# Kernel tuning notes

Hardware: AMD Instinct MI355X
Metric: run time of the kernel (lower is better)

## Reference

```python
import jax, jax.numpy as jnp
import numpy as np

D_MODEL = 1024
N_HEADS = 8
HEAD_DIM = D_MODEL // N_HEADS
B, T = 4, 2048


def setup_inputs() -> dict:
    key = jax.random.key(0)
    ks = jax.random.split(key, 10)
    x = jax.random.normal(ks[0], (B, T, D_MODEL), dtype=jnp.float32)
    # causal mask: True entries are masked (matches torch masked_fill semantics)
    mask = jnp.triu(jnp.ones((T, T), dtype=bool), k=1)

    def xavier(k, shape):
        fan_in, fan_out = shape[1], shape[0]
        lim = float(np.sqrt(6.0 / (fan_in + fan_out)))
        return jax.random.uniform(k, shape, jnp.float32, -lim, lim)

    Wq = xavier(ks[1], (D_MODEL, D_MODEL)); bq = jnp.zeros((D_MODEL,), jnp.float32)
    Wk = xavier(ks[2], (D_MODEL, D_MODEL)); bk = jnp.zeros((D_MODEL,), jnp.float32)
    Wv = xavier(ks[3], (D_MODEL, D_MODEL)); bv = jnp.zeros((D_MODEL,), jnp.float32)
    Wo = xavier(ks[4], (D_MODEL, D_MODEL)); bo = jnp.zeros((D_MODEL,), jnp.float32)
    return {"x": x, "mask": mask, "Wq": Wq, "bq": bq, "Wk": Wk, "bk": bk,
            "Wv": Wv, "bv": bv, "Wo": Wo, "bo": bo}


def reference(x, mask, Wq, bq, Wk, bk, Wv, bv, Wo, bo):
    Bsz, Tlen, _ = x.shape
    # torch Linear: y = x @ W.T + b
    Q = (x @ Wq.T + bq).reshape(Bsz, Tlen, N_HEADS, HEAD_DIM).transpose(0, 2, 1, 3)  # [B,H,T,Dh]
    K = (x @ Wk.T + bk).reshape(Bsz, Tlen, N_HEADS, HEAD_DIM).transpose(0, 2, 1, 3)  # [B,H,T,Dh]
    V_shared = x @ Wv.T + bv  # [B,T,D] shared across heads
    scale = 1.0 / jnp.sqrt(jnp.float32(HEAD_DIM))
    scores = jnp.einsum('bhqd,bhkd->bhqk', Q, K) * scale  # [B,H,T,T]
    scores = jnp.where(mask[None, None, :, :], jnp.float32(-1e9), scores)
    attn_per_head = jax.nn.softmax(scores, axis=-1)
    alpha_agg = attn_per_head.mean(axis=1)  # [B,T,T] head-averaged attention
    out = jnp.einsum('bqk,bkd->bqd', alpha_agg, V_shared) @ Wo.T + bo
    return out, alpha_agg
```

## Files before the change

### kernel.cpp

```cpp
#include <hip/hip_runtime.h>
#include <hip/hip_bf16.h>

#define D_MODEL 1024
#define NH 8
#define HD 128
#define BATCH 4
#define TSEQ 2048
#define MROWS (BATCH * TSEQ)

typedef __attribute__((ext_vector_type(8))) __bf16 bf16x8;
typedef __attribute__((ext_vector_type(4))) __bf16 bf16x4;
typedef __attribute__((ext_vector_type(4))) float f32x4;
typedef __attribute__((ext_vector_type(8))) unsigned short u16x8;

__device__ __forceinline__ void gload16(const void* g, void* lds) {
  __builtin_amdgcn_global_load_lds(
      (const __attribute__((address_space(1))) unsigned int*)g,
      (__attribute__((address_space(3))) unsigned int*)lds, 16, 0, 0);
}

__global__ __launch_bounds__(256) void cvt_f32_to_bf16(const float* __restrict__ in,
                                                       __bf16* __restrict__ out, int n4) {
  int i = blockIdx.x * 256 + threadIdx.x;
  if (i < n4) {
    float4 v = reinterpret_cast<const float4*>(in)[i];
    bf16x4 o;
    o[0] = (__bf16)v.x; o[1] = (__bf16)v.y; o[2] = (__bf16)v.z; o[3] = (__bf16)v.w;
    reinterpret_cast<bf16x4*>(out)[i] = o;
  }
}

template <bool BF16OUT, bool CAUSAL, bool AFP32>
__global__ __launch_bounds__(256) void gemm128(const void* __restrict__ Aip,
                                               const __bf16* __restrict__ Bp,
                                               const float* __restrict__ bias,
                                               void* __restrict__ Yp, int K, int ldy,
                                               size_t sA, size_t sB, size_t sY) {
  __shared__ __bf16 As[128 * 32];
  __shared__ __bf16 Bs[128 * 32];
  const int tid = threadIdx.x;
  const int w = tid >> 6, l = tid & 63;
  const int lr = l & 15, lg = l >> 4;
  const int m0 = blockIdx.y * 128, n0 = blockIdx.x * 128;
  const int z = blockIdx.z;
  const __bf16* Ab = AFP32 ? nullptr : (const __bf16*)Aip + z * sA;
  const float* Af = AFP32 ? (const float*)Aip + z * sA : nullptr;
  const __bf16* Bb = Bp + z * sB;
  const int wm = w >> 1, wn = w & 1;
  f32x4 acc[4][4] = {};
  const int Klim = CAUSAL ? (m0 + 128 < K ? m0 + 128 : K) : K;

  for (int k0 = 0; k0 < Klim; k0 += 32) {
    if (k0) __syncthreads();
    if constexpr (!AFP32) {
#pragma unroll
      for (int i = 0; i < 2; ++i) {
        int s = w * 128 + i * 64 + l;
        int row = s >> 2, scp = s & 3;
        int sc = scp ^ ((row >> 1) & 3);
        gload16(Ab + (size_t)(m0 + row) * K + k0 + sc * 8, (char*)As + s * 16);
      }
    } else {
#pragma unroll
      for (int i = 0; i < 2; ++i) {
        int s = w * 128 + i * 64 + l;
        int row = s >> 2, sc = s & 3;
        const float* src = Af + (size_t)(m0 + row) * K + k0 + sc * 8;
        float4 lo = *reinterpret_cast<const float4*>(src);
        float4 hi = *reinterpret_cast<const float4*>(src + 4);
        bf16x8 v;
        v[0] = (__bf16)lo.x; v[1] = (__bf16)lo.y; v[2] = (__bf16)lo.z; v[3] = (__bf16)lo.w;
        v[4] = (__bf16)hi.x; v[5] = (__bf16)hi.y; v[6] = (__bf16)hi.z; v[7] = (__bf16)hi.w;
        int p = row * 4 + (sc ^ ((row >> 1) & 3));
        *reinterpret_cast<bf16x8*>((char*)As + p * 16) = v;
      }
    }
#pragma unroll
    for (int i = 0; i < 2; ++i) {
      int s = w * 128 + i * 64 + l;
      int row = s >> 2, scp = s & 3;
      int sc = scp ^ ((row >> 1) & 3);
      gload16(Bb + (size_t)(n0 + row) * K + k0 + sc * 8, (char*)Bs + s * 16);
    }
    __syncthreads();
    bf16x8 af[4], bf[4];
#pragma unroll
    for (int f = 0; f < 4; ++f) {
      int ar = wm * 64 + f * 16 + lr;
      af[f] = *reinterpret_cast<const bf16x8*>((const char*)As + ar * 64 +
                                               ((lg ^ ((ar >> 1) & 3)) * 16));
      int br = wn * 64 + f * 16 + lr;
      bf[f] = *reinterpret_cast<const bf16x8*>((const char*)Bs + br * 64 +
                                               ((lg ^ ((br >> 1) & 3)) * 16));
    }
#pragma unroll
    for (int mf = 0; mf < 4; ++mf)
#pragma unroll
      for (int nf = 0; nf < 4; ++nf)
        acc[mf][nf] = __builtin_amdgcn_mfma_f32_16x16x32_bf16(af[mf], bf[nf], acc[mf][nf], 0, 0, 0);
  }

#pragma unroll
  for (int mf = 0; mf < 4; ++mf) {
#pragma unroll
    for (int nf = 0; nf < 4; ++nf) {
#pragma unroll
      for (int r = 0; r < 4; ++r) {
        int grow = m0 + wm * 64 + mf * 16 + lg * 4 + r;
        int gcol = n0 + wn * 64 + nf * 16 + lr;
        float v = acc[mf][nf][r];
        if (bias) v += bias[gcol];
        if constexpr (BF16OUT)
          ((__bf16*)Yp + z * sY)[(size_t)grow * ldy + gcol] = (__bf16)v;
        else
          ((float*)Yp + z * sY)[(size_t)grow * ldy + gcol] = v;
      }
    }
  }
}

__global__ __launch_bounds__(256) void transpose_v(const __bf16* __restrict__ V,
                                                   __bf16* __restrict__ Vt) {
  __shared__ unsigned short tile[64 * 72];
  const int b = blockIdx.z;
  const int t0 = blockIdx.x * 64, d0 = blockIdx.y * 64;
  const int tid = threadIdx.x;
#pragma unroll
  for (int i = 0; i < 2; ++i) {
    int s = i * 256 + tid;
    int r = s >> 3, c8 = s & 7;
    u16x8 v = *reinterpret_cast<const u16x8*>(V + ((size_t)b * TSEQ + t0 + r) * D_MODEL + d0 + c8 * 8);
    *reinterpret_cast<u16x8*>(&tile[r * 72 + c8 * 8]) = v;
  }
  __syncthreads();
#pragma unroll
  for (int i = 0; i < 2; ++i) {
    int s = i * 256 + tid;
    int dr = s >> 3, t8 = s & 7;
    u16x8 o;
#pragma unroll
    for (int j = 0; j < 8; ++j) o[j] = tile[(t8 * 8 + j) * 72 + dr];
    *reinterpret_cast<u16x8*>(Vt + ((size_t)b * D_MODEL + d0 + dr) * TSEQ + t0 + t8 * 8) = o;
  }
}

#define STAGE_QK(srcbase, dst)                                                    \
  {                                                                               \
    _Pragma("unroll") for (int i = 0; i < 4; ++i) {                               \
      int s = w * 256 + i * 64 + l;                                               \
      int row = s >> 4, sp = s & 15;                                              \
      int sc = sp ^ (row & 7);                                                    \
      gload16((srcbase) + (size_t)row * D_MODEL + sc * 8, (char*)(dst) + s * 16); \
    }                                                                             \
  }

__device__ __forceinline__ bf16x8 ld_tile(const __bf16* t, int row, int c, int lg) {
  return *reinterpret_cast<const bf16x8*>((const char*)t + row * 256 +
                                          (((c * 4 + lg) ^ (row & 7)) * 16));
}

__global__ __launch_bounds__(256) void attn_stats(const __bf16* __restrict__ Q,
                                                  const __bf16* __restrict__ Kp,
                                                  float* __restrict__ Linv) {
  __shared__ __bf16 Qs[64 * 128];
  __shared__ __bf16 Ks[64 * 128];
  const int tid = threadIdx.x;
  const int w = tid >> 6, l = tid & 63;
  const int lr = l & 15, lg = l >> 4;
  const int qt = blockIdx.x, q0 = qt * 64;
  const int b = blockIdx.y >> 3, h = blockIdx.y & 7;
  const float scale = 0.08838834764831845f;

  const __bf16* qsrc = Q + ((size_t)(b * TSEQ + q0)) * D_MODEL + h * HD;
  STAGE_QK(qsrc, Qs);

  bf16x8 af[4];
  float lsum[4] = {0.f, 0.f, 0.f, 0.f};
  const int nkt = qt + 1;
  for (int kt = 0; kt < nkt; ++kt) {
    if (kt) __syncthreads();
    const __bf16* ksrc = Kp + ((size_t)(b * TSEQ + kt * 64)) * D_MODEL + h * HD;
    STAGE_QK(ksrc, Ks);
    __syncthreads();
    if (kt == 0) {
      int qrow = w * 16 + lr;
#pragma unroll
      for (int c = 0; c < 4; ++c) af[c] = ld_tile(Qs, qrow, c, lg);
    }
#pragma unroll
    for (int kf = 0; kf < 4; ++kf) {
      f32x4 acc = {};
      int krow = kf * 16 + lr;
#pragma unroll
      for (int c = 0; c < 4; ++c)
        acc = __builtin_amdgcn_mfma_f32_16x16x32_bf16(af[c], ld_tile(Ks, krow, c, lg), acc, 0, 0, 0);
      if (kt == qt) {
#pragma unroll
        for (int r = 0; r < 4; ++r) {
          int q = q0 + w * 16 + lg * 4 + r;
          int k = kt * 64 + kf * 16 + lr;
          if (k <= q) lsum[r] += __expf(acc[r] * scale);
        }
      } else {
#pragma unroll
        for (int r = 0; r < 4; ++r) lsum[r] += __expf(acc[r] * scale);
      }
    }
  }
#pragma unroll
  for (int m = 1; m < 16; m <<= 1)
#pragma unroll
    for (int r = 0; r < 4; ++r) lsum[r] += __shfl_xor(lsum[r], m, 64);
  if (lr == 0) {
#pragma unroll
    for (int r = 0; r < 4; ++r)
      Linv[((size_t)(b * NH + h)) * TSEQ + q0 + w * 16 + lg * 4 + r] =
          1.0f / ((float)NH * lsum[r]);
  }
}

__global__ __launch_bounds__(256) void attn_alpha(const __bf16* __restrict__ Q,
                                                  const __bf16* __restrict__ Kp,
                                                  const float* __restrict__ Linv,
                                                  float* __restrict__ alpha) {
  const int kt = blockIdx.x, qt = blockIdx.y, b = blockIdx.z;
  const int q0 = qt * 64, k0 = kt * 64;
  const int tid = threadIdx.x;
  if (kt > qt) {
    float4 zz = {0.f, 0.f, 0.f, 0.f};
#pragma unroll
    for (int i = 0; i < 4; ++i) {
      int s = i * 256 + tid;
      int row = s >> 4, c4 = s & 15;
      *reinterpret_cast<float4*>(alpha + ((size_t)(b * TSEQ) + q0 + row) * TSEQ + k0 + c4 * 4) = zz;
    }
    return;
  }
  __shared__ __bf16 Qs[64 * 128];
  __shared__ __bf16 Ks[64 * 128];
  const int w = tid >> 6, l = tid & 63;
  const int lr = l & 15, lg = l >> 4;
  const float scale = 0.08838834764831845f;
  float outv[4][4] = {};

  for (int h = 0; h < NH; ++h) {
    if (h) __syncthreads();
    const __bf16* qsrc = Q + ((size_t)(b * TSEQ + q0)) * D_MODEL + h * HD;
    const __bf16* ksrc = Kp + ((size_t)(b * TSEQ + k0)) * D_MODEL + h * HD;
    STAGE_QK(qsrc, Qs);
    STAGE_QK(ksrc, Ks);
    __syncthreads();
    bf16x8 af[4];
    int qrow = w * 16 + lr;
#pragma unroll
    for (int c = 0; c < 4; ++c) af[c] = ld_tile(Qs, qrow, c, lg);
    float li[4];
#pragma unroll
    for (int r = 0; r < 4; ++r)
      li[r] = Linv[((size_t)(b * NH + h)) * TSEQ + q0 + w * 16 + lg * 4 + r];
#pragma unroll
    for (int kf = 0; kf < 4; ++kf) {
      f32x4 acc = {};
      int krow = kf * 16 + lr;
#pragma unroll
      for (int c = 0; c < 4; ++c)
        acc = __builtin_amdgcn_mfma_f32_16x16x32_bf16(af[c], ld_tile(Ks, krow, c, lg), acc, 0, 0, 0);
      if (kt == qt) {
#pragma unroll
        for (int r = 0; r < 4; ++r) {
          int q = q0 + w * 16 + lg * 4 + r;
          int k = k0 + kf * 16 + lr;
          if (k <= q) outv[kf][r] += __expf(acc[r] * scale) * li[r];
        }
      } else {
#pragma unroll
        for (int r = 0; r < 4; ++r) outv[kf][r] += __expf(acc[r] * scale) * li[r];
      }
    }
  }
#pragma unroll
  for (int kf = 0; kf < 4; ++kf)
#pragma unroll
    for (int r = 0; r < 4; ++r)
      alpha[((size_t)(b * TSEQ) + q0 + w * 16 + lg * 4 + r) * TSEQ + k0 + kf * 16 + lr] =
          outv[kf][r];
}

extern "C" void kernel_launch(void* const* d_in, const int* in_sizes, int n_in,
                              void* d_out, int out_size, void* d_ws, size_t ws_size,
                              hipStream_t stream) {
  const float* x  = (const float*)d_in[0];
  const float* Wq = (const float*)d_in[2];
  const float* bq = (const float*)d_in[3];
  const float* Wk = (const float*)d_in[4];
  const float* bk = (const float*)d_in[5];
  const float* Wv = (const float*)d_in[6];
  const float* bv = (const float*)d_in[7];
  const float* Wo = (const float*)d_in[8];
  const float* bo = (const float*)d_in[9];

  float* out_f = (float*)d_out;
  float* alpha = out_f + (size_t)MROWS * D_MODEL;

  char* p = (char*)d_ws;
  __bf16* xb  = (__bf16*)p; p += (size_t)MROWS * D_MODEL * 2;
  __bf16* wqb = (__bf16*)p; p += (size_t)D_MODEL * D_MODEL * 2;
  __bf16* wkb = (__bf16*)p; p += (size_t)D_MODEL * D_MODEL * 2;
  __bf16* wvb = (__bf16*)p; p += (size_t)D_MODEL * D_MODEL * 2;
  __bf16* wob = (__bf16*)p; p += (size_t)D_MODEL * D_MODEL * 2;
  __bf16* qb  = (__bf16*)p; p += (size_t)MROWS * D_MODEL * 2;
  __bf16* kb  = (__bf16*)p; p += (size_t)MROWS * D_MODEL * 2;
  __bf16* vb  = (__bf16*)p; p += (size_t)MROWS * D_MODEL * 2;
  __bf16* vtb = (__bf16*)p; p += (size_t)BATCH * D_MODEL * TSEQ * 2;
  float* linv = (float*)p;  p += (size_t)BATCH * NH * TSEQ * 4;
  __bf16* midb = xb;

  {
    int n4 = MROWS * D_MODEL / 4;
    cvt_f32_to_bf16<<<n4 / 256, 256, 0, stream>>>(x, xb, n4);
    int w4 = D_MODEL * D_MODEL / 4;
    cvt_f32_to_bf16<<<w4 / 256, 256, 0, stream>>>(Wq, wqb, w4);
    cvt_f32_to_bf16<<<w4 / 256, 256, 0, stream>>>(Wk, wkb, w4);
    cvt_f32_to_bf16<<<w4 / 256, 256, 0, stream>>>(Wv, wvb, w4);
    cvt_f32_to_bf16<<<w4 / 256, 256, 0, stream>>>(Wo, wob, w4);
  }

  dim3 pgrid(D_MODEL / 128, MROWS / 128, 1);
  gemm128<true, false, false><<<pgrid, 256, 0, stream>>>(xb, wqb, bq, qb, D_MODEL, D_MODEL, 0, 0, 0);
  gemm128<true, false, false><<<pgrid, 256, 0, stream>>>(xb, wkb, bk, kb, D_MODEL, D_MODEL, 0, 0, 0);
  gemm128<true, false, false><<<pgrid, 256, 0, stream>>>(xb, wvb, bv, vb, D_MODEL, D_MODEL, 0, 0, 0);

  transpose_v<<<dim3(TSEQ / 64, D_MODEL / 64, BATCH), 256, 0, stream>>>(vb, vtb);

  attn_stats<<<dim3(TSEQ / 64, BATCH * NH), 256, 0, stream>>>(qb, kb, linv);

  attn_alpha<<<dim3(TSEQ / 64, TSEQ / 64, BATCH), 256, 0, stream>>>(qb, kb, linv, alpha);

  gemm128<true, true, true><<<dim3(D_MODEL / 128, TSEQ / 128, BATCH), 256, 0, stream>>>(
      alpha, vtb, nullptr, midb, TSEQ, D_MODEL,
      (size_t)TSEQ * TSEQ, (size_t)D_MODEL * TSEQ, (size_t)TSEQ * D_MODEL);

  gemm128<false, false, false><<<pgrid, 256, 0, stream>>>(midb, wob, bo, out_f, D_MODEL, D_MODEL, 0, 0, 0);
}
```

Measured before the change: 350.9 us.

## Double-buffer GEMM and attention tiles, retile warps 2x2, fuse weight conversions

The GEMM and both attention kernels now double-buffer their LDS tiles, so the next tile's global loads are issued while MFMAs run on the current one. The attention kernels split the 64x64 tile across warps in a 2x2 layout with a wider XOR swizzle, and use exp2f with a prescaled constant. The four weight-conversion launches are merged into one kernel. The cost is doubled LDS use, which may lower occupancy, plus an extra LDS reduction step in attn_stats.

```diff
diff --git a/kernel.cpp b/kernel.cpp
--- a/kernel.cpp
+++ b/kernel.cpp
@@ -12,6 +12,8 @@
 typedef __attribute__((ext_vector_type(4))) __bf16 bf16x4;
 typedef __attribute__((ext_vector_type(4))) float f32x4;
 typedef __attribute__((ext_vector_type(8))) unsigned short u16x8;
+
+#define SC2 0.1275174441680632f
 
 __device__ __forceinline__ void gload16(const void* g, void* lds) {
   __builtin_amdgcn_global_load_lds(
@@ -30,14 +32,29 @@
   }
 }
 
+__global__ __launch_bounds__(256) void cvt4_weights(const float* __restrict__ w0,
+                                                    const float* __restrict__ w1,
+                                                    const float* __restrict__ w2,
+                                                    const float* __restrict__ w3,
+                                                    __bf16* __restrict__ out) {
+  const int per = D_MODEL * D_MODEL / 4;
+  int i = blockIdx.x * 256 + threadIdx.x;
+  int m = i / per, j = i - m * per;
+  const float* src = (m == 0) ? w0 : (m == 1) ? w1 : (m == 2) ? w2 : w3;
+  float4 v = reinterpret_cast<const float4*>(src)[j];
+  bf16x4 o;
+  o[0] = (__bf16)v.x; o[1] = (__bf16)v.y; o[2] = (__bf16)v.z; o[3] = (__bf16)v.w;
+  reinterpret_cast<bf16x4*>(out)[i] = o;
+}
+
 template <bool BF16OUT, bool CAUSAL, bool AFP32>
 __global__ __launch_bounds__(256) void gemm128(const void* __restrict__ Aip,
                                                const __bf16* __restrict__ Bp,
                                                const float* __restrict__ bias,
                                                void* __restrict__ Yp, int K, int ldy,
                                                size_t sA, size_t sB, size_t sY) {
-  __shared__ __bf16 As[128 * 32];
-  __shared__ __bf16 Bs[128 * 32];
+  __shared__ __bf16 As[2][128 * 32];
+  __shared__ __bf16 Bs[2][128 * 32];
   const int tid = threadIdx.x;
   const int w = tid >> 6, l = tid & 63;
   const int lr = l & 15, lg = l >> 4;
@@ -49,16 +66,17 @@
   const int wm = w >> 1, wn = w & 1;
   f32x4 acc[4][4] = {};
   const int Klim = CAUSAL ? (m0 + 128 < K ? m0 + 128 : K) : K;
-
-  for (int k0 = 0; k0 < Klim; k0 += 32) {
-    if (k0) __syncthreads();
+  const int nt = Klim >> 5;
+
+  auto stage = [&](int t, int buf) {
+    const int k0 = t << 5;
     if constexpr (!AFP32) {
 #pragma unroll
       for (int i = 0; i < 2; ++i) {
         int s = w * 128 + i * 64 + l;
         int row = s >> 2, scp = s & 3;
         int sc = scp ^ ((row >> 1) & 3);
-        gload16(Ab + (size_t)(m0 + row) * K + k0 + sc * 8, (char*)As + s * 16);
+        gload16(Ab + (size_t)(m0 + row) * K + k0 + sc * 8, (char*)As[buf] + s * 16);
       }
     } else {
 #pragma unroll
@@ -72,7 +90,7 @@
         v[0] = (__bf16)lo.x; v[1] = (__bf16)lo.y; v[2] = (__bf16)lo.z; v[3] = (__bf16)lo.w;
         v[4] = (__bf16)hi.x; v[5] = (__bf16)hi.y; v[6] = (__bf16)hi.z; v[7] = (__bf16)hi.w;
         int p = row * 4 + (sc ^ ((row >> 1) & 3));
-        *reinterpret_cast<bf16x8*>((char*)As + p * 16) = v;
+        *reinterpret_cast<bf16x8*>((char*)As[buf] + p * 16) = v;
       }
     }
 #pragma unroll
@@ -80,17 +98,23 @@
       int s = w * 128 + i * 64 + l;
       int row = s >> 2, scp = s & 3;
       int sc = scp ^ ((row >> 1) & 3);
-      gload16(Bb + (size_t)(n0 + row) * K + k0 + sc * 8, (char*)Bs + s * 16);
-    }
-    __syncthreads();
+      gload16(Bb + (size_t)(n0 + row) * K + k0 + sc * 8, (char*)Bs[buf] + s * 16);
+    }
+  };
+
+  stage(0, 0);
+  __syncthreads();
+  int cur = 0;
+  for (int t = 0; t < nt; ++t) {
+    if (t + 1 < nt) stage(t + 1, cur ^ 1);
     bf16x8 af[4], bf[4];
 #pragma unroll
     for (int f = 0; f < 4; ++f) {
       int ar = wm * 64 + f * 16 + lr;
-      af[f] = *reinterpret_cast<const bf16x8*>((const char*)As + ar * 64 +
+      af[f] = *reinterpret_cast<const bf16x8*>((const char*)As[cur] + ar * 64 +
                                                ((lg ^ ((ar >> 1) & 3)) * 16));
       int br = wn * 64 + f * 16 + lr;
-      bf[f] = *reinterpret_cast<const bf16x8*>((const char*)Bs + br * 64 +
+      bf[f] = *reinterpret_cast<const bf16x8*>((const char*)Bs[cur] + br * 64 +
                                                ((lg ^ ((br >> 1) & 3)) * 16));
     }
 #pragma unroll
@@ -98,6 +122,8 @@
 #pragma unroll
       for (int nf = 0; nf < 4; ++nf)
         acc[mf][nf] = __builtin_amdgcn_mfma_f32_16x16x32_bf16(af[mf], bf[nf], acc[mf][nf], 0, 0, 0);
+    __syncthreads();
+    cur ^= 1;
   }
 
 #pragma unroll
@@ -144,78 +170,101 @@
   }
 }
 
-#define STAGE_QK(srcbase, dst)                                                    \
-  {                                                                               \
-    _Pragma("unroll") for (int i = 0; i < 4; ++i) {                               \
-      int s = w * 256 + i * 64 + l;                                               \
-      int row = s >> 4, sp = s & 15;                                              \
-      int sc = sp ^ (row & 7);                                                    \
-      gload16((srcbase) + (size_t)row * D_MODEL + sc * 8, (char*)(dst) + s * 16); \
-    }                                                                             \
-  }
-
-__device__ __forceinline__ bf16x8 ld_tile(const __bf16* t, int row, int c, int lg) {
+#define STAGE_T(srcbase, dst)                                                      \
+  {                                                                                \
+    _Pragma("unroll") for (int i = 0; i < 4; ++i) {                                \
+      int s = i * 256 + tid;                                                       \
+      int row = s >> 4, sp = s & 15;                                               \
+      int sl = sp ^ (row & 15);                                                    \
+      gload16((srcbase) + (size_t)row * D_MODEL + sl * 8, (char*)(dst) + s * 16);  \
+    }                                                                              \
+  }
+
+__device__ __forceinline__ bf16x8 ldfrag(const __bf16* t, int row, int c, int lg) {
   return *reinterpret_cast<const bf16x8*>((const char*)t + row * 256 +
-                                          (((c * 4 + lg) ^ (row & 7)) * 16));
+                                          (((c * 4 + lg) ^ (row & 15)) * 16));
 }
 
 __global__ __launch_bounds__(256) void attn_stats(const __bf16* __restrict__ Q,
                                                   const __bf16* __restrict__ Kp,
                                                   float* __restrict__ Linv) {
   __shared__ __bf16 Qs[64 * 128];
-  __shared__ __bf16 Ks[64 * 128];
+  __shared__ __bf16 Ks[2][64 * 128];
+  __shared__ float Lred[2][64];
   const int tid = threadIdx.x;
   const int w = tid >> 6, l = tid & 63;
   const int lr = l & 15, lg = l >> 4;
+  const int wq = w >> 1, wk = w & 1;
   const int qt = blockIdx.x, q0 = qt * 64;
   const int b = blockIdx.y >> 3, h = blockIdx.y & 7;
-  const float scale = 0.08838834764831845f;
 
   const __bf16* qsrc = Q + ((size_t)(b * TSEQ + q0)) * D_MODEL + h * HD;
-  STAGE_QK(qsrc, Qs);
-
-  bf16x8 af[4];
-  float lsum[4] = {0.f, 0.f, 0.f, 0.f};
-  const int nkt = qt + 1;
-  for (int kt = 0; kt < nkt; ++kt) {
-    if (kt) __syncthreads();
-    const __bf16* ksrc = Kp + ((size_t)(b * TSEQ + kt * 64)) * D_MODEL + h * HD;
-    STAGE_QK(ksrc, Ks);
+  const __bf16* kbase = Kp + ((size_t)b * TSEQ) * D_MODEL + h * HD;
+  STAGE_T(qsrc, Qs);
+  STAGE_T(kbase, Ks[0]);
+  __syncthreads();
+
+  bf16x8 af[2][4];
+#pragma unroll
+  for (int mf = 0; mf < 2; ++mf)
+#pragma unroll
+    for (int c = 0; c < 4; ++c) af[mf][c] = ldfrag(Qs, wq * 32 + mf * 16 + lr, c, lg);
+
+  float lsum[2][4] = {};
+  int cur = 0;
+  for (int kt = 0; kt <= qt; ++kt) {
+    if (kt < qt) STAGE_T(kbase + (size_t)(kt + 1) * 64 * D_MODEL, Ks[cur ^ 1]);
+    bf16x8 bfr[2][4];
+#pragma unroll
+    for (int nf = 0; nf < 2; ++nf)
+#pragma unroll
+      for (int c = 0; c < 4; ++c) bfr[nf][c] = ldfrag(Ks[cur], wk * 32 + nf * 16 + lr, c, lg);
+    f32x4 acc[2][2] = {};
+#pragma unroll
+    for (int c = 0; c < 4; ++c)
+#pragma unroll
+      for (int mf = 0; mf < 2; ++mf)
+#pragma unroll
+        for (int nf = 0; nf < 2; ++nf)
+          acc[mf][nf] = __builtin_amdgcn_mfma_f32_16x16x32_bf16(af[mf][c], bfr[nf][c], acc[mf][nf], 0, 0, 0);
+    if (kt == qt) {
+#pragma unroll
+      for (int mf = 0; mf < 2; ++mf)
+#pragma unroll
+        for (int nf = 0; nf < 2; ++nf)
+#pragma unroll
+          for (int r = 0; r < 4; ++r) {
+            int q = q0 + wq * 32 + mf * 16 + lg * 4 + r;
+            int k = kt * 64 + wk * 32 + nf * 16 + lr;
+            if (k <= q) lsum[mf][r] += exp2f(acc[mf][nf][r] * SC2);
+          }
+    } else {
+#pragma unroll
+      for (int mf = 0; mf < 2; ++mf)
+#pragma unroll
+        for (int nf = 0; nf < 2; ++nf)
+#pragma unroll
+          for (int r = 0; r < 4; ++r) lsum[mf][r] += exp2f(acc[mf][nf][r] * SC2);
+    }
     __syncthreads();
-    if (kt == 0) {
-      int qrow = w * 16 + lr;
-#pragma unroll
-      for (int c = 0; c < 4; ++c) af[c] = ld_tile(Qs, qrow, c, lg);
-    }
-#pragma unroll
-    for (int kf = 0; kf < 4; ++kf) {
-      f32x4 acc = {};
-      int krow = kf * 16 + lr;
-#pragma unroll
-      for (int c = 0; c < 4; ++c)
-        acc = __builtin_amdgcn_mfma_f32_16x16x32_bf16(af[c], ld_tile(Ks, krow, c, lg), acc, 0, 0, 0);
-      if (kt == qt) {
-#pragma unroll
-        for (int r = 0; r < 4; ++r) {
-          int q = q0 + w * 16 + lg * 4 + r;
-          int k = kt * 64 + kf * 16 + lr;
-          if (k <= q) lsum[r] += __expf(acc[r] * scale);
-        }
-      } else {
-#pragma unroll
-        for (int r = 0; r < 4; ++r) lsum[r] += __expf(acc[r] * scale);
-      }
-    }
+    cur ^= 1;
   }
 #pragma unroll
   for (int m = 1; m < 16; m <<= 1)
 #pragma unroll
-    for (int r = 0; r < 4; ++r) lsum[r] += __shfl_xor(lsum[r], m, 64);
+    for (int mf = 0; mf < 2; ++mf)
+#pragma unroll
+      for (int r = 0; r < 4; ++r) lsum[mf][r] += __shfl_xor(lsum[mf][r], m, 64);
   if (lr == 0) {
 #pragma unroll
-    for (int r = 0; r < 4; ++r)
-      Linv[((size_t)(b * NH + h)) * TSEQ + q0 + w * 16 + lg * 4 + r] =
-          1.0f / ((float)NH * lsum[r]);
+    for (int mf = 0; mf < 2; ++mf)
+#pragma unroll
+      for (int r = 0; r < 4; ++r) Lred[wk][wq * 32 + mf * 16 + lg * 4 + r] = lsum[mf][r];
+  }
+  __syncthreads();
+  if (tid < 64) {
+    float s = Lred[0][tid] + Lred[1][tid];
+    Linv[((size_t)(b * NH + h)) * TSEQ + q0 + tid] = 1.0f / (8.0f * s);
   }
 }
 
@@ -236,54 +285,78 @@
     }
     return;
   }
-  __shared__ __bf16 Qs[64 * 128];
-  __shared__ __bf16 Ks[64 * 128];
+  __shared__ __bf16 Qs[2][64 * 128];
+  __shared__ __bf16 Ks[2][64 * 128];
   const int w = tid >> 6, l = tid & 63;
   const int lr = l & 15, lg = l >> 4;
-  const float scale = 0.08838834764831845f;
-  float outv[4][4] = {};
-
+  const int wq = w >> 1, wk = w & 1;
+  const __bf16* qb0 = Q + ((size_t)(b * TSEQ + q0)) * D_MODEL;
+  const __bf16* kb0 = Kp + ((size_t)(b * TSEQ + k0)) * D_MODEL;
+  float outv[2][2][4] = {};
+
+  STAGE_T(qb0, Qs[0]);
+  STAGE_T(kb0, Ks[0]);
+  __syncthreads();
+  int cur = 0;
   for (int h = 0; h < NH; ++h) {
-    if (h) __syncthreads();
-    const __bf16* qsrc = Q + ((size_t)(b * TSEQ + q0)) * D_MODEL + h * HD;
-    const __bf16* ksrc = Kp + ((size_t)(b * TSEQ + k0)) * D_MODEL + h * HD;
-    STAGE_QK(qsrc, Qs);
-    STAGE_QK(ksrc, Ks);
+    if (h + 1 < NH) {
+      STAGE_T(qb0 + (h + 1) * HD, Qs[cur ^ 1]);
+      STAGE_T(kb0 + (h + 1) * HD, Ks[cur ^ 1]);
+    }
+    bf16x8 af[2][4], bfr[2][4];
+#pragma unroll
+    for (int mf = 0; mf < 2; ++mf)
+#pragma unroll
+      for (int c = 0; c < 4; ++c) af[mf][c] = ldfrag(Qs[cur], wq * 32 + mf * 16 + lr, c, lg);
+#pragma unroll
+    for (int nf = 0; nf < 2; ++nf)
+#pragma unroll
+      for (int c = 0; c < 4; ++c) bfr[nf][c] = ldfrag(Ks[cur], wk * 32 + nf * 16 + lr, c, lg);
+    f32x4 acc[2][2] = {};
+#pragma unroll
+    for (int c = 0; c < 4; ++c)
+#pragma unroll
+      for (int mf = 0; mf < 2; ++mf)
+#pragma unroll
+        for (int nf = 0; nf < 2; ++nf)
+          acc[mf][nf] = __builtin_amdgcn_mfma_f32_16x16x32_bf16(af[mf][c], bfr[nf][c], acc[mf][nf], 0, 0, 0);
+    float4 li[2];
+#pragma unroll
+    for (int mf = 0; mf < 2; ++mf)
+      li[mf] = *reinterpret_cast<const float4*>(
+          &Linv[((size_t)(b * NH + h)) * TSEQ + q0 + wq * 32 + mf * 16 + lg * 4]);
+    if (kt == qt) {
+#pragma unroll
+      for (int mf = 0; mf < 2; ++mf)
+#pragma unroll
+        for (int nf = 0; nf < 2; ++nf)
+#pragma unroll
+          for (int r = 0; r < 4; ++r) {
+            int q = q0 + wq * 32 + mf * 16 + lg * 4 + r;
+            int k = k0 + wk * 32 + nf * 16 + lr;
+            if (k <= q)
+              outv[mf][nf][r] += exp2f(acc[mf][nf][r] * SC2) * (&li[mf].x)[r];
+          }
+    } else {
+#pragma unroll
+      for (int mf = 0; mf < 2; ++mf)
+#pragma unroll
+        for (int nf = 0; nf < 2; ++nf)
+#pragma unroll
+          for (int r = 0; r < 4; ++r)
+            outv[mf][nf][r] += exp2f(acc[mf][nf][r] * SC2) * (&li[mf].x)[r];
+    }
     __syncthreads();
-    bf16x8 af[4];
-    int qrow = w * 16 + lr;
-#pragma unroll
-    for (int c = 0; c < 4; ++c) af[c] = ld_tile(Qs, qrow, c, lg);
-    float li[4];
-#pragma unroll
-    for (int r = 0; r < 4; ++r)
-      li[r] = Linv[((size_t)(b * NH + h)) * TSEQ + q0 + w * 16 + lg * 4 + r];
-#pragma unroll
-    for (int kf = 0; kf < 4; ++kf) {
-      f32x4 acc = {};
-      int krow = kf * 16 + lr;
-#pragma unroll
-      for (int c = 0; c < 4; ++c)
-        acc = __builtin_amdgcn_mfma_f32_16x16x32_bf16(af[c], ld_tile(Ks, krow, c, lg), acc, 0, 0, 0);
-      if (kt == qt) {
-#pragma unroll
-        for (int r = 0; r < 4; ++r) {
-          int q = q0 + w * 16 + lg * 4 + r;
-          int k = k0 + kf * 16 + lr;
-          if (k <= q) outv[kf][r] += __expf(acc[r] * scale) * li[r];
-        }
-      } else {
-#pragma unroll
-        for (int r = 0; r < 4; ++r) outv[kf][r] += __expf(acc[r] * scale) * li[r];
-      }
-    }
-  }
-#pragma unroll
-  for (int kf = 0; kf < 4; ++kf)
-#pragma unroll
-    for (int r = 0; r < 4; ++r)
-      alpha[((size_t)(b * TSEQ) + q0 + w * 16 + lg * 4 + r) * TSEQ + k0 + kf * 16 + lr] =
-          outv[kf][r];
+    cur ^= 1;
+  }
+#pragma unroll
+  for (int mf = 0; mf < 2; ++mf)
+#pragma unroll
+    for (int nf = 0; nf < 2; ++nf)
+#pragma unroll
+      for (int r = 0; r < 4; ++r)
+        alpha[((size_t)(b * TSEQ) + q0 + wq * 32 + mf * 16 + lg * 4 + r) * TSEQ +
+              k0 + wk * 32 + nf * 16 + lr] = outv[mf][nf][r];
 }
 
 extern "C" void kernel_launch(void* const* d_in, const int* in_sizes, int n_in,
@@ -318,11 +391,8 @@
   {
     int n4 = MROWS * D_MODEL / 4;
     cvt_f32_to_bf16<<<n4 / 256, 256, 0, stream>>>(x, xb, n4);
-    int w4 = D_MODEL * D_MODEL / 4;
-    cvt_f32_to_bf16<<<w4 / 256, 256, 0, stream>>>(Wq, wqb, w4);
-    cvt_f32_to_bf16<<<w4 / 256, 256, 0, stream>>>(Wk, wkb, w4);
-    cvt_f32_to_bf16<<<w4 / 256, 256, 0, stream>>>(Wv, wvb, w4);
-    cvt_f32_to_bf16<<<w4 / 256, 256, 0, stream>>>(Wo, wob, w4);
+    int w4 = 4 * D_MODEL * D_MODEL / 4;
+    cvt4_weights<<<w4 / 256, 256, 0, stream>>>(Wq, Wk, Wv, Wo, wqb);
   }
 
   dim3 pgrid(D_MODEL / 128, MROWS / 128, 1);
```

New measurement: 381.3 us. +8.6%, slower.
